# Kernel optimization log

Measured on AMD Instinct MI355X. Metric: run time of the kernel, lower is better.

## Reference

```python
import jax, jax.numpy as jnp
import numpy as np

N_NODES = 20000
N_EDGES = 320000
N_GRAPHS = 128
IN_CH = 64
DIM = 32
NEG_SLOPE = 0.2
EPS = 1e-16


def _gat_conv(x, src, dst, W, att_src, att_dst, bias, heads, ch):
    """PyG GATConv (concat=True, self-loops already included in src/dst).
    x: [N, F_in]; W: [heads*ch, F_in]; att_*: [heads, ch]; bias: [heads*ch].
    Returns [N, heads*ch]."""
    N = x.shape[0]
    h = (x @ W.T).reshape(N, heads, ch)                      # [N, H, C]
    a_src = (h * att_src[None]).sum(-1)                      # [N, H]
    a_dst = (h * att_dst[None]).sum(-1)                      # [N, H]
    e = jax.nn.leaky_relu(a_src[src] + a_dst[dst], NEG_SLOPE)  # [E, H]
    # segment softmax over edges sharing a destination node
    m = jax.ops.segment_max(e, dst, num_segments=N)          # [N, H]
    ex = jnp.exp(e - m[dst])
    s = jax.ops.segment_sum(ex, dst, num_segments=N)
    alpha = ex / (s[dst] + EPS)                              # [E, H]
    msg = alpha[:, :, None] * h[src]                         # [E, H, C]
    out = jax.ops.segment_sum(msg, dst, num_segments=N)      # [N, H, C]
    return out.reshape(N, heads * ch) + bias[None, :]


def setup_inputs() -> dict:
    key = jax.random.key(0)
    ks = jax.random.split(key, 20)

    x = jax.random.normal(ks[0], (N_NODES, IN_CH), dtype=jnp.float32)
    edge_index = jax.random.randint(ks[1], (2, N_EDGES), 0, N_NODES, dtype=jnp.int64)
    batch = jnp.sort(jax.random.randint(ks[2], (N_NODES,), 0, N_GRAPHS, dtype=jnp.int64))

    def lin_init(k, shape, fan_in):
        return jax.random.normal(k, shape, dtype=jnp.float32) * (1.0 / np.sqrt(fan_in))

    H1, C1 = 5, DIM * 2      # conv1: in -> dim*2, heads 5 -> out dim*10
    H2, C2 = 5, DIM * 3      # conv2: dim*10 -> dim*3, heads 5 -> out dim*15
    H3, C3 = 1, DIM          # conv3: dim*15 -> dim, heads 1

    inp = {
        "x": x,
        "W1": lin_init(ks[3], (H1 * C1, IN_CH), IN_CH),
        "att_src1": lin_init(ks[4], (H1, C1), C1),
        "att_dst1": lin_init(ks[5], (H1, C1), C1),
        "b1": jnp.zeros((H1 * C1,), jnp.float32),
        "W2": lin_init(ks[6], (H2 * C2, H1 * C1), H1 * C1),
        "att_src2": lin_init(ks[7], (H2, C2), C2),
        "att_dst2": lin_init(ks[8], (H2, C2), C2),
        "b2": jnp.zeros((H2 * C2,), jnp.float32),
        "W3": lin_init(ks[9], (H3 * C3, H2 * C2), H2 * C2),
        "att_src3": lin_init(ks[10], (H3, C3), C3),
        "att_dst3": lin_init(ks[11], (H3, C3), C3),
        "b3": jnp.zeros((H3 * C3,), jnp.float32),
        "lin_w": lin_init(ks[12], (1024, DIM), DIM),
        "lin_b": jnp.zeros((1024,), jnp.float32),
        "lin2_w": lin_init(ks[13], (1, 1024), 1024),
        "lin2_b": jnp.zeros((1,), jnp.float32),
        "edge_index": edge_index,
        "batch": batch,
    }
    return inp


def reference(x, W1, att_src1, att_dst1, b1,
              W2, att_src2, att_dst2, b2,
              W3, att_src3, att_dst3, b3,
              lin_w, lin_b, lin2_w, lin2_b,
              edge_index, batch):
    N = x.shape[0]
    # PyG GATConv adds self-loops by default
    loops = jnp.arange(N, dtype=edge_index.dtype)
    src = jnp.concatenate([edge_index[0], loops])
    dst = jnp.concatenate([edge_index[1], loops])

    h = _gat_conv(x, src, dst, W1, att_src1, att_dst1, b1, 5, DIM * 2)
    h = jax.nn.relu(h)                                   # dropout p=0 -> identity
    h = _gat_conv(h, src, dst, W2, att_src2, att_dst2, b2, 5, DIM * 3)
    h = jax.nn.relu(h)
    h = _gat_conv(h, src, dst, W3, att_src3, att_dst3, b3, 1, DIM)
    h = jax.nn.relu(h)

    g = jax.ops.segment_sum(h, batch, num_segments=N_GRAPHS)   # global_add_pool [G, dim]
    g = jax.nn.relu(g @ lin_w.T + lin_b[None, :])
    g = g @ lin2_w.T + lin2_b[None, :]
    return jax.nn.sigmoid(g)                                   # [G, out_channels]
```

## Files before the change

kernel.cpp:

```cpp
#include <hip/hip_runtime.h>
#include <math.h>

#define NN 20000
#define NE 320000
#define NG 128

typedef short short8 __attribute__((ext_vector_type(8)));
typedef float f32x4 __attribute__((ext_vector_type(4)));
typedef float f32x2 __attribute__((ext_vector_type(2)));
typedef unsigned short ushort;
typedef unsigned short ushort4v __attribute__((ext_vector_type(4)));
typedef float float4v __attribute__((ext_vector_type(4)));
typedef unsigned int uint;
typedef unsigned int uint2v __attribute__((ext_vector_type(2)));

__device__ __forceinline__ float b2f(ushort u) {
    unsigned int v = ((unsigned int)u) << 16;
    return __uint_as_float(v);
}
__device__ __forceinline__ ushort f2b(float f) {
    unsigned int u = __float_as_uint(f);
    u = (u + 0x7fff + ((u >> 16) & 1)) >> 16;
    return (ushort)u;
}
__device__ __forceinline__ float lrelu(float x) { return x >= 0.f ? x : 0.2f * x; }
__device__ __forceinline__ unsigned char f2f8(float v) {
    return (unsigned char)(__builtin_amdgcn_cvt_pk_fp8_f32(v, v, 0, false) & 0xff);
}
__device__ __forceinline__ void dec8(uint2v r, f32x2 d[4]) {
    d[0] = __builtin_amdgcn_cvt_pk_f32_fp8(r.x, false);
    d[1] = __builtin_amdgcn_cvt_pk_f32_fp8(r.x, true);
    d[2] = __builtin_amdgcn_cvt_pk_f32_fp8(r.y, false);
    d[3] = __builtin_amdgcn_cvt_pk_f32_fp8(r.y, true);
}

#define CVT_N0 (NN * 64 / 4)
#define CVT_N1 (320 * 64 / 4)
#define CVT_N2 (480 * 320 / 4)
#define CVT_N3 (32 * 480 / 4)
__global__ void f2b4_kernel(const float* __restrict__ a0, ushort* __restrict__ o0,
                            const float* __restrict__ a1, ushort* __restrict__ o1,
                            const float* __restrict__ a2, ushort* __restrict__ o2,
                            const float* __restrict__ a3, ushort* __restrict__ o3) {
    int i = blockIdx.x * blockDim.x + threadIdx.x;
    const float* src; ushort* dst; int li;
    if (i < CVT_N0) { src = a0; dst = o0; li = i; }
    else if (i < CVT_N0 + CVT_N1) { src = a1; dst = o1; li = i - CVT_N0; }
    else if (i < CVT_N0 + CVT_N1 + CVT_N2) { src = a2; dst = o2; li = i - CVT_N0 - CVT_N1; }
    else if (i < CVT_N0 + CVT_N1 + CVT_N2 + CVT_N3) { src = a3; dst = o3; li = i - CVT_N0 - CVT_N1 - CVT_N2; }
    else return;
    float4v v = *(const float4v*)(src + (size_t)li * 4);
    ushort4v r;
    r.x = f2b(v.x); r.y = f2b(v.y); r.z = f2b(v.z); r.w = f2b(v.w);
    *(ushort4v*)(dst + (size_t)li * 4) = r;
}

__global__ void count_kernel(const int* __restrict__ dst, int* __restrict__ cnt, int E) {
    int i = blockIdx.x * blockDim.x + threadIdx.x;
    if (i < E) atomicAdd(&cnt[dst[i]], 1);
}

__global__ __launch_bounds__(1024) void scan_kernel(const int* __restrict__ cnt,
                                                    int* __restrict__ row_start, int n) {
    __shared__ int sh[1024];
    int tid = threadIdx.x;
    int base = tid * 20;
    int local[20];
    int s = 0;
    #pragma unroll
    for (int k = 0; k < 20; ++k) {
        int idx = base + k;
        int v = (idx < n) ? cnt[idx] : 0;
        local[k] = s;
        s += v;
    }
    sh[tid] = s;
    __syncthreads();
    for (int off = 1; off < 1024; off <<= 1) {
        int t = (tid >= off) ? sh[tid - off] : 0;
        __syncthreads();
        sh[tid] += t;
        __syncthreads();
    }
    int pre = (tid == 0) ? 0 : sh[tid - 1];
    #pragma unroll
    for (int k = 0; k < 20; ++k) {
        int idx = base + k;
        if (idx < n) row_start[idx] = pre + local[k];
    }
    if (tid == 1023) row_start[n] = sh[1023];
}

__global__ void fill_kernel(const int* __restrict__ src, const int* __restrict__ dst,
                            const int* __restrict__ row_start, int* __restrict__ cursor,
                            int* __restrict__ csr_src, int E) {
    int i = blockIdx.x * blockDim.x + threadIdx.x;
    if (i < E) {
        int d = dst[i];
        int pos = atomicAdd(&cursor[d], 1);
        csr_src[row_start[d] + pos] = src[i];
    }
}

template <int K, int NF, int H, bool F8>
__global__ __launch_bounds__(256) void gemm_lds(const ushort* __restrict__ A,
                                                const ushort* __restrict__ B,
                                                ushort* __restrict__ C,
                                                unsigned char* __restrict__ C8,
                                                const float* __restrict__ att_src,
                                                const float* __restrict__ att_dst,
                                                float* __restrict__ a_src,
                                                float* __restrict__ a_dst,
                                                int M, int N, int gridx) {
    constexpr int BN = NF * 16;
    constexpr int KC = (K % 160 == 0) ? 160 : K;
    constexpr int NCHK = K / KC;
    constexpr int KS = KC / 32;
    __shared__ ushort Bs[BN][KC + 8];

    const int nwg = gridDim.x;
    int bid = blockIdx.x;
    {
        int q = nwg >> 3, r = nwg & 7;
        int xcd = bid & 7, idx = bid >> 3;
        bid = (xcd < r ? xcd * (q + 1) : r * (q + 1) + (xcd - r) * q) + idx;
    }
    const int by = bid / gridx;
    const int bx = bid % gridx;
    const int bn = bx * BN;

    const int tid = threadIdx.x;
    const int w = tid >> 6;
    const int lane = tid & 63;
    const int l15 = lane & 15;
    const int lhi = lane >> 4;

    const int bm = by * 64 + w * 16;
    int arow = bm + l15;
    if (arow >= M) arow = M - 1;
    const ushort* ap = A + (size_t)arow * K + lhi * 8;

    f32x4 acc[NF];
    #pragma unroll
    for (int f = 0; f < NF; ++f) acc[f] = (f32x4){0.f, 0.f, 0.f, 0.f};

    #pragma unroll
    for (int ch = 0; ch < NCHK; ++ch) {
        const int c0 = ch * KC;
        if (ch > 0) __syncthreads();
        constexpr int NCH = BN * (KC / 8);
        for (int i = tid; i < NCH; i += 256) {
            int r = i / (KC / 8), c8 = i % (KC / 8);
            short8 v = *(const short8*)(B + (size_t)(bn + r) * K + c0 + c8 * 8);
            *(short8*)(&Bs[r][c8 * 8]) = v;
        }
        __syncthreads();

        short8 a_cur = *(const short8*)(ap + c0);
        short8 b_cur[NF], b_nxt[NF];
        #pragma unroll
        for (int f = 0; f < NF; ++f)
            b_cur[f] = *(const short8*)(&Bs[f * 16 + l15][lhi * 8]);

        #pragma unroll
        for (int ks = 0; ks < KS; ++ks) {
            short8 a_nxt = a_cur;
            if (ks + 1 < KS) {
                a_nxt = *(const short8*)(ap + c0 + (ks + 1) * 32);
                #pragma unroll
                for (int f = 0; f < NF; ++f)
                    b_nxt[f] = *(const short8*)(&Bs[f * 16 + l15][(ks + 1) * 32 + lhi * 8]);
            }
            #pragma unroll
            for (int f = 0; f < NF; ++f)
                acc[f] = __builtin_amdgcn_mfma_f32_16x16x32_bf16(a_cur, b_cur[f], acc[f], 0, 0, 0);
            a_cur = a_nxt;
            #pragma unroll
            for (int f = 0; f < NF; ++f) b_cur[f] = b_nxt[f];
        }
    }

    #pragma unroll
    for (int f = 0; f < NF; ++f) {
        #pragma unroll
        for (int j = 0; j < 4; ++j) {
            int row = bm + lhi * 4 + j;
            if (row < M) {
                if (F8) C8[(size_t)row * N + bn + f * 16 + l15] = f2f8(acc[f][j]);
                else    C[(size_t)row * N + bn + f * 16 + l15] = f2b(acc[f][j]);
            }
        }
    }

    float as_v[NF], ad_v[NF];
    #pragma unroll
    for (int f = 0; f < NF; ++f) {
        as_v[f] = att_src[bx * BN + f * 16 + l15];
        ad_v[f] = att_dst[bx * BN + f * 16 + l15];
    }
    #pragma unroll
    for (int j = 0; j < 4; ++j) {
        float ps = 0.f, pd = 0.f;
        #pragma unroll
        for (int f = 0; f < NF; ++f) {
            ps += acc[f][j] * as_v[f];
            pd += acc[f][j] * ad_v[f];
        }
        #pragma unroll
        for (int off = 1; off < 16; off <<= 1) {
            ps += __shfl_xor(ps, off);
            pd += __shfl_xor(pd, off);
        }
        int row = bm + lhi * 4 + j;
        if (l15 == 0 && row < M) {
            a_src[row * H + bx] = ps;
            a_dst[row * H + bx] = pd;
        }
    }
}

template <int H, int C>
__global__ void gat_agg_f8(const unsigned char* __restrict__ h8,
                           const float* __restrict__ a_src, const float* __restrict__ a_dst,
                           const int* __restrict__ row_start, const int* __restrict__ csr_src,
                           const float* __restrict__ bias, ushort* __restrict__ out, int N) {
    constexpr int W = H * C;
    constexpr int VL = W / 8;
    int n = (blockIdx.x * blockDim.x + threadIdx.x) >> 6;
    int lane = threadIdx.x & 63;
    if (n >= N) return;
    bool act = lane < VL;
    int l = act ? lane : 0;
    int hd = (8 * l) / C;
    float adst = a_dst[n * H + hd];

    float m = lrelu(a_src[n * H + hd] + adst);
    float ssum = 1.f;
    f32x2 acc2[4];
    {
        uint2v r = *(const uint2v*)(h8 + (size_t)n * W + 8 * l);
        dec8(r, acc2);
    }

    int rs = row_start[n], re = row_start[n + 1];
    int i = rs;
    for (; i + 8 <= re; i += 8) {
        int s[8]; uint2v r[8]; float e[8];
        #pragma unroll
        for (int j = 0; j < 8; ++j) s[j] = csr_src[i + j];
        #pragma unroll
        for (int j = 0; j < 8; ++j) r[j] = *(const uint2v*)(h8 + (size_t)s[j] * W + 8 * l);
        #pragma unroll
        for (int j = 0; j < 8; ++j) e[j] = lrelu(a_src[s[j] * H + hd] + adst);
        float nm = m;
        #pragma unroll
        for (int j = 0; j < 8; ++j) nm = fmaxf(nm, e[j]);
        float scale = __expf(m - nm);
        m = nm;
        f32x2 sc = {scale, scale};
        #pragma unroll
        for (int d = 0; d < 4; ++d) acc2[d] *= sc;
        ssum *= scale;
        float wsum = 0.f;
        #pragma unroll
        for (int j = 0; j < 8; ++j) {
            float wj = __expf(e[j] - nm);
            wsum += wj;
            f32x2 dd[4];
            dec8(r[j], dd);
            f32x2 vw = {wj, wj};
            #pragma unroll
            for (int d = 0; d < 4; ++d) acc2[d] += vw * dd[d];
        }
        ssum += wsum;
    }
    for (; i + 4 <= re; i += 4) {
        int s[4]; uint2v r[4]; float e[4];
        #pragma unroll
        for (int j = 0; j < 4; ++j) s[j] = csr_src[i + j];
        #pragma unroll
        for (int j = 0; j < 4; ++j) r[j] = *(const uint2v*)(h8 + (size_t)s[j] * W + 8 * l);
        #pragma unroll
        for (int j = 0; j < 4; ++j) e[j] = lrelu(a_src[s[j] * H + hd] + adst);
        float nm = m;
        #pragma unroll
        for (int j = 0; j < 4; ++j) nm = fmaxf(nm, e[j]);
        float scale = __expf(m - nm);
        m = nm;
        f32x2 sc = {scale, scale};
        #pragma unroll
        for (int d = 0; d < 4; ++d) acc2[d] *= sc;
        ssum *= scale;
        float wsum = 0.f;
        #pragma unroll
        for (int j = 0; j < 4; ++j) {
            float wj = __expf(e[j] - nm);
            wsum += wj;
            f32x2 dd[4];
            dec8(r[j], dd);
            f32x2 vw = {wj, wj};
            #pragma unroll
            for (int d = 0; d < 4; ++d) acc2[d] += vw * dd[d];
        }
        ssum += wsum;
    }
    for (; i < re; ++i) {
        int s = csr_src[i];
        uint2v r = *(const uint2v*)(h8 + (size_t)s * W + 8 * l);
        float e = lrelu(a_src[s * H + hd] + adst);
        float nm = fmaxf(m, e);
        float scale = __expf(m - nm);
        m = nm;
        float wgt = __expf(e - nm);
        ssum = ssum * scale + wgt;
        f32x2 dd[4];
        dec8(r, dd);
        f32x2 sc = {scale, scale};
        f32x2 vw = {wgt, wgt};
        #pragma unroll
        for (int d = 0; d < 4; ++d) acc2[d] = acc2[d] * sc + vw * dd[d];
    }

    float inv = 1.f / (ssum + 1e-16f);
    if (act) {
        short8 o;
        #pragma unroll
        for (int d = 0; d < 4; ++d) {
            #pragma unroll
            for (int e2 = 0; e2 < 2; ++e2) {
                float v = acc2[d][e2] * inv + bias[8 * l + 2 * d + e2];
                o[2 * d + e2] = (short)f2b(v > 0.f ? v : 0.f);
            }
        }
        *(short8*)(out + (size_t)n * W + 8 * l) = o;
    }
}

__global__ void gat_agg_c32(const ushort* __restrict__ h, const float* __restrict__ a_src,
                            const float* __restrict__ a_dst, const int* __restrict__ row_start,
                            const int* __restrict__ csr_src, const float* __restrict__ bias,
                            ushort* __restrict__ out, int N) {
    int n = (blockIdx.x * blockDim.x + threadIdx.x) >> 6;
    int lane = threadIdx.x & 63;
    if (n >= N) return;
    int g = lane >> 2;
    int q = lane & 3;
    float adst = a_dst[n];
    int rs = row_start[n];
    int total = row_start[n + 1] - rs + 1;

    float m = -1e30f, ssum = 0.f;
    float acc[8];
    #pragma unroll
    for (int j = 0; j < 8; ++j) acc[j] = 0.f;

    for (int k = g; k < total; k += 16) {
        int s = (k == 0) ? n : csr_src[rs + k - 1];
        float e = lrelu(a_src[s] + adst);
        float nm = fmaxf(m, e);
        float scale = __expf(m - nm);
        m = nm;
        float w = __expf(e - nm);
        ssum = ssum * scale + w;
        short8 r = *(const short8*)(h + (size_t)s * 32 + 8 * q);
        #pragma unroll
        for (int j = 0; j < 8; ++j) acc[j] = acc[j] * scale + w * b2f((ushort)r[j]);
    }

    #pragma unroll
    for (int off = 4; off < 64; off <<= 1) {
        float m2 = __shfl_xor(m, off);
        float s2 = __shfl_xor(ssum, off);
        float nm = fmaxf(m, m2);
        float sc1 = __expf(m - nm), sc2 = __expf(m2 - nm);
        ssum = ssum * sc1 + s2 * sc2;
        #pragma unroll
        for (int j = 0; j < 8; ++j) {
            float a2 = __shfl_xor(acc[j], off);
            acc[j] = acc[j] * sc1 + a2 * sc2;
        }
        m = nm;
    }

    if (lane < 4) {
        float inv = 1.f / (ssum + 1e-16f);
        short8 o;
        #pragma unroll
        for (int j = 0; j < 8; ++j) {
            float v = acc[j] * inv + bias[8 * lane + j];
            o[j] = (short)f2b(v > 0.f ? v : 0.f);
        }
        *(short8*)(out + (size_t)n * 32 + 8 * lane) = o;
    }
}

__global__ __launch_bounds__(256) void pool_graph(const ushort* __restrict__ x,
                                                  const int* __restrict__ batch,
                                                  float* __restrict__ g, int N) {
    int gr = blockIdx.x;
    int a = 0, b = N;
    while (a < b) { int mid = (a + b) >> 1; if (batch[mid] < gr) a = mid + 1; else b = mid; }
    int lo = a;
    b = N;
    while (a < b) { int mid = (a + b) >> 1; if (batch[mid] < gr + 1) a = mid + 1; else b = mid; }
    int hi = a;

    int tid = threadIdx.x;
    int c = tid & 31;
    int grp = tid >> 5;
    float s = 0.f;
    for (int n = lo + grp; n < hi; n += 8)
        s += b2f(x[(size_t)n * 32 + c]);
    __shared__ float sh[8][33];
    sh[grp][c] = s;
    __syncthreads();
    if (tid < 32) {
        float t = 0.f;
        #pragma unroll
        for (int k = 0; k < 8; ++k) t += sh[k][c];
        g[gr * 32 + c] = t;
    }
}

__global__ __launch_bounds__(256) void mlp_fused(const float* __restrict__ gpool,
                                                 const float* __restrict__ lin_w,
                                                 const float* __restrict__ lin_b,
                                                 const float* __restrict__ lin2_w,
                                                 const float* __restrict__ lin2_b,
                                                 float* __restrict__ outp) {
    int gr = blockIdx.x;
    int tid = threadIdx.x;
    __shared__ float grow[32];
    __shared__ float red[4];
    if (tid < 8) {
        float4v v = *(const float4v*)(gpool + gr * 32 + tid * 4);
        *(float4v*)(&grow[tid * 4]) = v;
    }
    __syncthreads();
    float partial = 0.f;
    #pragma unroll
    for (int u = 0; u < 4; ++u) {
        int o = tid + u * 256;
        float s = lin_b[o];
        const float* wp = lin_w + (size_t)o * 32;
        #pragma unroll
        for (int k = 0; k < 32; ++k) s += grow[k] * wp[k];
        s = s > 0.f ? s : 0.f;
        partial += s * lin2_w[o];
    }
    #pragma unroll
    for (int off = 32; off; off >>= 1) partial += __shfl_down(partial, off);
    int lane = tid & 63, wv = tid >> 6;
    if (lane == 0) red[wv] = partial;
    __syncthreads();
    if (tid == 0) {
        float t = red[0] + red[1] + red[2] + red[3] + lin2_b[0];
        outp[gr] = 1.f / (1.f + expf(-t));
    }
}

static inline size_t al256(size_t x) { return (x + 255) & ~(size_t)255; }

extern "C" void kernel_launch(void* const* d_in, const int* in_sizes, int n_in,
                              void* d_out, int out_size, void* d_ws, size_t ws_size,
                              hipStream_t stream) {
    const float* x      = (const float*)d_in[0];
    const float* W1     = (const float*)d_in[1];
    const float* as1    = (const float*)d_in[2];
    const float* ad1    = (const float*)d_in[3];
    const float* b1     = (const float*)d_in[4];
    const float* W2     = (const float*)d_in[5];
    const float* as2    = (const float*)d_in[6];
    const float* ad2    = (const float*)d_in[7];
    const float* b2     = (const float*)d_in[8];
    const float* W3     = (const float*)d_in[9];
    const float* as3    = (const float*)d_in[10];
    const float* ad3    = (const float*)d_in[11];
    const float* b3     = (const float*)d_in[12];
    const float* lin_w  = (const float*)d_in[13];
    const float* lin_b  = (const float*)d_in[14];
    const float* lin2_w = (const float*)d_in[15];
    const float* lin2_b = (const float*)d_in[16];
    const int*   ei     = (const int*)d_in[17];
    const int*   batch  = (const int*)d_in[18];
    float* outp = (float*)d_out;

    const int E = in_sizes[17] / 2;
    const int* e_src = ei;
    const int* e_dst = ei + E;

    char* p = (char*)d_ws;
    ushort* h_bf   = (ushort*)p; p += al256((size_t)NN * 480 * 2);
    ushort* o_bf   = (ushort*)p; p += al256((size_t)NN * 480 * 2);
    unsigned char* h_f8 = (unsigned char*)p; p += al256((size_t)NN * 480);
    ushort* x_bf   = (ushort*)p; p += al256((size_t)NN * 64 * 2);
    ushort* w1_bf  = (ushort*)p; p += al256((size_t)320 * 64 * 2);
    ushort* w2_bf  = (ushort*)p; p += al256((size_t)480 * 320 * 2);
    ushort* w3_bf  = (ushort*)p; p += al256((size_t)32 * 480 * 2);
    float* asrc    = (float*)p; p += al256((size_t)NN * 5 * 4);
    float* adst    = (float*)p; p += al256((size_t)NN * 5 * 4);
    int*   row_st  = (int*)p;   p += al256((size_t)(NN + 1) * 4);
    int*   cnt     = (int*)p;   p += (size_t)NN * 4;
    int*   cursor  = (int*)p;   p += (size_t)NN * 4;
    p = (char*)al256((size_t)p);
    int*   csr_src = (int*)p;   p += al256((size_t)NE * 4);
    float* gpool   = (float*)p; p += al256((size_t)NG * 32 * 4);
    (void)ws_size; (void)n_in; (void)out_size;

    dim3 blk(256);

    hipMemsetAsync(cnt, 0, (size_t)2 * NN * 4, stream);
    count_kernel<<<(E + 255) / 256, 256, 0, stream>>>(e_dst, cnt, E);
    scan_kernel<<<1, 1024, 0, stream>>>(cnt, row_st, NN);
    fill_kernel<<<(E + 255) / 256, 256, 0, stream>>>(e_src, e_dst, row_st, cursor, csr_src, E);

    {
        int tot = CVT_N0 + CVT_N1 + CVT_N2 + CVT_N3;
        f2b4_kernel<<<(tot + 255) / 256, blk, 0, stream>>>(x, x_bf, W1, w1_bf, W2, w2_bf, W3, w3_bf);
    }

    const int MPAN = (NN + 63) / 64;
    const int NBLK = (NN + 3) / 4;
    {
        gemm_lds<64, 4, 5, true><<<5 * MPAN, blk, 0, stream>>>(x_bf, w1_bf, h_bf, h_f8, as1, ad1, asrc, adst, NN, 320, 5);
        gat_agg_f8<5, 64><<<NBLK, blk, 0, stream>>>(h_f8, asrc, adst, row_st, csr_src, b1, o_bf, NN);
    }
    {
        gemm_lds<320, 6, 5, true><<<5 * MPAN, blk, 0, stream>>>(o_bf, w2_bf, h_bf, h_f8, as2, ad2, asrc, adst, NN, 480, 5);
        gat_agg_f8<5, 96><<<NBLK, blk, 0, stream>>>(h_f8, asrc, adst, row_st, csr_src, b2, o_bf, NN);
    }
    {
        gemm_lds<480, 2, 1, false><<<1 * MPAN, blk, 0, stream>>>(o_bf, w3_bf, h_bf, h_f8, as3, ad3, asrc, adst, NN, 32, 1);
        gat_agg_c32<<<NBLK, blk, 0, stream>>>(h_bf, asrc, adst, row_st, csr_src, b3, o_bf, NN);
    }
    pool_graph<<<NG, blk, 0, stream>>>(o_bf, batch, gpool, NN);
    mlp_fused<<<NG, blk, 0, stream>>>(gpool, lin_w, lin_b, lin2_w, lin2_b, outp);
}
```

Before: 194.2 us.

## Fuse conversion with edge count, pool with MLP, and flatten layer-1 aggregation

Merges the bf16 conversion kernel with the destination-count kernel, and merges graph pooling with the MLP head, removing two launches and the intermediate pooled buffer. Adds a flat-indexed layer-1 aggregation kernel that maps 40 threads per node, where the old kernel used a 64-lane wavefront per node and left lanes idle. Also drops the 4-wide unrolled tail from the layer-2 aggregator. The cost is more divergent, non-wave-aligned node groups and a larger scalar tail loop in layer 2.

```diff
diff --git a/kernel.cpp b/kernel.cpp
--- a/kernel.cpp
+++ b/kernel.cpp
@@ -38,26 +38,24 @@
 #define CVT_N1 (320 * 64 / 4)
 #define CVT_N2 (480 * 320 / 4)
 #define CVT_N3 (32 * 480 / 4)
-__global__ void f2b4_kernel(const float* __restrict__ a0, ushort* __restrict__ o0,
-                            const float* __restrict__ a1, ushort* __restrict__ o1,
-                            const float* __restrict__ a2, ushort* __restrict__ o2,
-                            const float* __restrict__ a3, ushort* __restrict__ o3) {
+#define CVT_TOT (CVT_N0 + CVT_N1 + CVT_N2 + CVT_N3)
+__global__ void cvt_count_kernel(const float* __restrict__ a0, ushort* __restrict__ o0,
+                                 const float* __restrict__ a1, ushort* __restrict__ o1,
+                                 const float* __restrict__ a2, ushort* __restrict__ o2,
+                                 const float* __restrict__ a3, ushort* __restrict__ o3,
+                                 const int* __restrict__ e_dst, int* __restrict__ cnt, int E) {
     int i = blockIdx.x * blockDim.x + threadIdx.x;
+    if (i < E) atomicAdd(&cnt[e_dst[i]], 1);
     const float* src; ushort* dst; int li;
     if (i < CVT_N0) { src = a0; dst = o0; li = i; }
     else if (i < CVT_N0 + CVT_N1) { src = a1; dst = o1; li = i - CVT_N0; }
     else if (i < CVT_N0 + CVT_N1 + CVT_N2) { src = a2; dst = o2; li = i - CVT_N0 - CVT_N1; }
-    else if (i < CVT_N0 + CVT_N1 + CVT_N2 + CVT_N3) { src = a3; dst = o3; li = i - CVT_N0 - CVT_N1 - CVT_N2; }
+    else if (i < CVT_TOT) { src = a3; dst = o3; li = i - CVT_N0 - CVT_N1 - CVT_N2; }
     else return;
     float4v v = *(const float4v*)(src + (size_t)li * 4);
     ushort4v r;
     r.x = f2b(v.x); r.y = f2b(v.y); r.z = f2b(v.z); r.w = f2b(v.w);
     *(ushort4v*)(dst + (size_t)li * 4) = r;
-}
-
-__global__ void count_kernel(const int* __restrict__ dst, int* __restrict__ cnt, int E) {
-    int i = blockIdx.x * blockDim.x + threadIdx.x;
-    if (i < E) atomicAdd(&cnt[dst[i]], 1);
 }
 
 __global__ __launch_bounds__(1024) void scan_kernel(const int* __restrict__ cnt,
@@ -220,6 +218,90 @@
 }
 
 template <int H, int C>
+__global__ void gat_agg_f8_flat(const unsigned char* __restrict__ h8,
+                                const float* __restrict__ a_src, const float* __restrict__ a_dst,
+                                const int* __restrict__ row_start, const int* __restrict__ csr_src,
+                                const float* __restrict__ bias, ushort* __restrict__ out, int N) {
+    constexpr int W = H * C;
+    constexpr int NCHK = W / 8;
+    int t = blockIdx.x * blockDim.x + threadIdx.x;
+    int n = t / NCHK;
+    int l = t % NCHK;
+    if (n >= N) return;
+    int hd = (8 * l) / C;
+    float adst = a_dst[n * H + hd];
+
+    float m = lrelu(a_src[n * H + hd] + adst);
+    float ssum = 1.f;
+    f32x2 acc2[4];
+    {
+        uint2v r = *(const uint2v*)(h8 + (size_t)n * W + 8 * l);
+        dec8(r, acc2);
+    }
+
+    int rs = row_start[n], re = row_start[n + 1];
+    int i = rs;
+    for (; i + 8 <= re; i += 8) {
+        int s[8]; uint2v r[8]; float e[8];
+        #pragma unroll
+        for (int j = 0; j < 8; ++j) s[j] = csr_src[i + j];
+        #pragma unroll
+        for (int j = 0; j < 8; ++j) r[j] = *(const uint2v*)(h8 + (size_t)s[j] * W + 8 * l);
+        #pragma unroll
+        for (int j = 0; j < 8; ++j) e[j] = lrelu(a_src[s[j] * H + hd] + adst);
+        float nm = m;
+        #pragma unroll
+        for (int j = 0; j < 8; ++j) nm = fmaxf(nm, e[j]);
+        float scale = __expf(m - nm);
+        m = nm;
+        f32x2 sc = {scale, scale};
+        #pragma unroll
+        for (int d = 0; d < 4; ++d) acc2[d] *= sc;
+        ssum *= scale;
+        float wsum = 0.f;
+        #pragma unroll
+        for (int j = 0; j < 8; ++j) {
+            float wj = __expf(e[j] - nm);
+            wsum += wj;
+            f32x2 dd[4];
+            dec8(r[j], dd);
+            f32x2 vw = {wj, wj};
+            #pragma unroll
+            for (int d = 0; d < 4; ++d) acc2[d] += vw * dd[d];
+        }
+        ssum += wsum;
+    }
+    for (; i < re; ++i) {
+        int s = csr_src[i];
+        uint2v r = *(const uint2v*)(h8 + (size_t)s * W + 8 * l);
+        float e = lrelu(a_src[s * H + hd] + adst);
+        float nm = fmaxf(m, e);
+        float scale = __expf(m - nm);
+        m = nm;
+        float wgt = __expf(e - nm);
+        ssum = ssum * scale + wgt;
+        f32x2 dd[4];
+        dec8(r, dd);
+        f32x2 sc = {scale, scale};
+        f32x2 vw = {wgt, wgt};
+        #pragma unroll
+        for (int d = 0; d < 4; ++d) acc2[d] = acc2[d] * sc + vw * dd[d];
+    }
+
+    float inv = 1.f / (ssum + 1e-16f);
+    short8 o;
+    #pragma unroll
+    for (int d = 0; d < 4; ++d) {
+        #pragma unroll
+        for (int e2 = 0; e2 < 2; ++e2) {
+            float v = acc2[d][e2] * inv + bias[8 * l + 2 * d + e2];
+            o[2 * d + e2] = (short)f2b(v > 0.f ? v : 0.f);
+        }
+    }
+    *(short8*)(out + (size_t)n * W + 8 * l) = o;
+}
+
+template <int H, int C>
 __global__ void gat_agg_f8(const unsigned char* __restrict__ h8,
                            const float* __restrict__ a_src, const float* __restrict__ a_dst,
                            const int* __restrict__ row_start, const int* __restrict__ csr_src,
@@ -274,36 +356,6 @@
         }
         ssum += wsum;
     }
-    for (; i + 4 <= re; i += 4) {
-        int s[4]; uint2v r[4]; float e[4];
-        #pragma unroll
-        for (int j = 0; j < 4; ++j) s[j] = csr_src[i + j];
-        #pragma unroll
-        for (int j = 0; j < 4; ++j) r[j] = *(const uint2v*)(h8 + (size_t)s[j] * W + 8 * l);
-        #pragma unroll
-        for (int j = 0; j < 4; ++j) e[j] = lrelu(a_src[s[j] * H + hd] + adst);
-        float nm = m;
-        #pragma unroll
-        for (int j = 0; j < 4; ++j) nm = fmaxf(nm, e[j]);
-        float scale = __expf(m - nm);
-        m = nm;
-        f32x2 sc = {scale, scale};
-        #pragma unroll
-        for (int d = 0; d < 4; ++d) acc2[d] *= sc;
-        ssum *= scale;
-        float wsum = 0.f;
-        #pragma unroll
-        for (int j = 0; j < 4; ++j) {
-            float wj = __expf(e[j] - nm);
-            wsum += wj;
-            f32x2 dd[4];
-            dec8(r[j], dd);
-            f32x2 vw = {wj, wj};
-            #pragma unroll
-            for (int d = 0; d < 4; ++d) acc2[d] += vw * dd[d];
-        }
-        ssum += wsum;
-    }
     for (; i < re; ++i) {
         int s = csr_src[i];
         uint2v r = *(const uint2v*)(h8 + (size_t)s * W + 8 * l);
@@ -394,9 +446,13 @@
     }
 }
 
-__global__ __launch_bounds__(256) void pool_graph(const ushort* __restrict__ x,
-                                                  const int* __restrict__ batch,
-                                                  float* __restrict__ g, int N) {
+__global__ __launch_bounds__(256) void pool_mlp(const ushort* __restrict__ x,
+                                                const int* __restrict__ batch,
+                                                const float* __restrict__ lin_w,
+                                                const float* __restrict__ lin_b,
+                                                const float* __restrict__ lin2_w,
+                                                const float* __restrict__ lin2_b,
+                                                float* __restrict__ outp, int N) {
     int gr = blockIdx.x;
     int a = 0, b = N;
     while (a < b) { int mid = (a + b) >> 1; if (batch[mid] < gr) a = mid + 1; else b = mid; }
@@ -412,41 +468,27 @@
     for (int n = lo + grp; n < hi; n += 8)
         s += b2f(x[(size_t)n * 32 + c]);
     __shared__ float sh[8][33];
+    __shared__ float grow[32];
+    __shared__ float red[4];
     sh[grp][c] = s;
     __syncthreads();
     if (tid < 32) {
         float t = 0.f;
         #pragma unroll
-        for (int k = 0; k < 8; ++k) t += sh[k][c];
-        g[gr * 32 + c] = t;
-    }
-}
-
-__global__ __launch_bounds__(256) void mlp_fused(const float* __restrict__ gpool,
-                                                 const float* __restrict__ lin_w,
-                                                 const float* __restrict__ lin_b,
-                                                 const float* __restrict__ lin2_w,
-                                                 const float* __restrict__ lin2_b,
-                                                 float* __restrict__ outp) {
-    int gr = blockIdx.x;
-    int tid = threadIdx.x;
-    __shared__ float grow[32];
-    __shared__ float red[4];
-    if (tid < 8) {
-        float4v v = *(const float4v*)(gpool + gr * 32 + tid * 4);
-        *(float4v*)(&grow[tid * 4]) = v;
+        for (int k = 0; k < 8; ++k) t += sh[k][tid];
+        grow[tid] = t;
     }
     __syncthreads();
     float partial = 0.f;
     #pragma unroll
     for (int u = 0; u < 4; ++u) {
         int o = tid + u * 256;
-        float s = lin_b[o];
+        float s2 = lin_b[o];
         const float* wp = lin_w + (size_t)o * 32;
         #pragma unroll
-        for (int k = 0; k < 32; ++k) s += grow[k] * wp[k];
-        s = s > 0.f ? s : 0.f;
-        partial += s * lin2_w[o];
+        for (int k = 0; k < 32; ++k) s2 += grow[k] * wp[k];
+        s2 = s2 > 0.f ? s2 : 0.f;
+        partial += s2 * lin2_w[o];
     }
     #pragma unroll
     for (int off = 32; off; off >>= 1) partial += __shfl_down(partial, off);
@@ -504,26 +546,25 @@
     int*   cursor  = (int*)p;   p += (size_t)NN * 4;
     p = (char*)al256((size_t)p);
     int*   csr_src = (int*)p;   p += al256((size_t)NE * 4);
-    float* gpool   = (float*)p; p += al256((size_t)NG * 32 * 4);
     (void)ws_size; (void)n_in; (void)out_size;
 
     dim3 blk(256);
 
     hipMemsetAsync(cnt, 0, (size_t)2 * NN * 4, stream);
-    count_kernel<<<(E + 255) / 256, 256, 0, stream>>>(e_dst, cnt, E);
+    {
+        int tot = CVT_TOT > NE ? CVT_TOT : NE;
+        cvt_count_kernel<<<(tot + 255) / 256, blk, 0, stream>>>(
+            x, x_bf, W1, w1_bf, W2, w2_bf, W3, w3_bf, e_dst, cnt, E);
+    }
     scan_kernel<<<1, 1024, 0, stream>>>(cnt, row_st, NN);
     fill_kernel<<<(E + 255) / 256, 256, 0, stream>>>(e_src, e_dst, row_st, cursor, csr_src, E);
 
-    {
-        int tot = CVT_N0 + CVT_N1 + CVT_N2 + CVT_N3;
-        f2b4_kernel<<<(tot + 255) / 256, blk, 0, stream>>>(x, x_bf, W1, w1_bf, W2, w2_bf, W3, w3_bf);
-    }
-
     const int MPAN = (NN + 63) / 64;
     const int NBLK = (NN + 3) / 4;
     {
         gemm_lds<64, 4, 5, true><<<5 * MPAN, blk, 0, stream>>>(x_bf, w1_bf, h_bf, h_f8, as1, ad1, asrc, adst, NN, 320, 5);
-        gat_agg_f8<5, 64><<<NBLK, blk, 0, stream>>>(h_f8, asrc, adst, row_st, csr_src, b1, o_bf, NN);
+        int tthr = NN * 40;
+        gat_agg_f8_flat<5, 64><<<(tthr + 255) / 256, blk, 0, stream>>>(h_f8, asrc, adst, row_st, csr_src, b1, o_bf, NN);
     }
     {
         gemm_lds<320, 6, 5, true><<<5 * MPAN, blk, 0, stream>>>(o_bf, w2_bf, h_bf, h_f8, as2, ad2, asrc, adst, NN, 480, 5);
@@ -533,6 +574,5 @@
         gemm_lds<480, 2, 1, false><<<1 * MPAN, blk, 0, stream>>>(o_bf, w3_bf, h_bf, h_f8, as3, ad3, asrc, adst, NN, 32, 1);
         gat_agg_c32<<<NBLK, blk, 0, stream>>>(h_bf, asrc, adst, row_st, csr_src, b3, o_bf, NN);
     }
-    pool_graph<<<NG, blk, 0, stream>>>(o_bf, batch, gpool, NN);
-    mlp_fused<<<NG, blk, 0, stream>>>(gpool, lin_w, lin_b, lin2_w, lin2_b, outp);
-}
+    pool_mlp<<<NG, blk, 0, stream>>>(o_bf, batch, lin_w, lin_b, lin2_w, lin2_b, outp, NN);
+}
```

New measurement: 191.3 us. About the same (-1.5%).
